# Optimization experiments

Measured on AMD Instinct MI355X. Metric: run time of the kernel, lower is better.

## Reference

```python
import jax, jax.numpy as jnp
import numpy as np

N_NODES = 50000
N_EDGES = 800000
F_IN, C1, C2, H = 256, 64, 64, 3
NEG_SLOPE = 0.2


def gat_layer(x, src, dst, W, a_src, a_dst, b, concat, num_nodes):
    """PyG-style GATConv. src/dst already include self-loops.
    W: [H*C, F_in], a_src/a_dst: [H, C], b: [H*C] or [C]."""
    H_, C_ = a_src.shape
    h = (x @ W.T).reshape(num_nodes, H_, C_)            # [N,H,C]
    al_src = (h * a_src).sum(-1)                        # [N,H]
    al_dst = (h * a_dst).sum(-1)                        # [N,H]
    e = jax.nn.leaky_relu(al_src[src] + al_dst[dst], NEG_SLOPE)  # [E,H]
    # segment softmax over incoming edges of each target node
    emax = jax.ops.segment_max(e, dst, num_segments=num_nodes)   # [N,H]
    ex = jnp.exp(e - emax[dst])
    denom = jax.ops.segment_sum(ex, dst, num_segments=num_nodes)  # [N,H]
    alpha = ex / (denom[dst] + 1e-16)                   # [E,H]
    msg = h[src] * alpha[:, :, None]                    # [E,H,C]
    out = jax.ops.segment_sum(msg, dst, num_segments=num_nodes)   # [N,H,C]
    if concat:
        return out.reshape(num_nodes, H_ * C_) + b
    return out.mean(axis=1) + b


def setup_inputs() -> dict:
    key = jax.random.key(0)
    ks = jax.random.split(key, 12)
    s = 0.05
    return {
        "x": jax.random.normal(ks[0], (N_NODES, F_IN), jnp.float32),
        "edge_index": jax.random.randint(ks[1], (2, N_EDGES), 0, N_NODES, jnp.int32),
        "W1": jax.random.normal(ks[2], (H * C1, F_IN), jnp.float32) * s,
        "a1_src": jax.random.normal(ks[3], (H, C1), jnp.float32) * s,
        "a1_dst": jax.random.normal(ks[4], (H, C1), jnp.float32) * s,
        "b1": jnp.zeros((H * C1,), jnp.float32),
        "W_mu": jax.random.normal(ks[5], (H * C2, H * C1), jnp.float32) * s,
        "a_mu_src": jax.random.normal(ks[6], (H, C2), jnp.float32) * s,
        "a_mu_dst": jax.random.normal(ks[7], (H, C2), jnp.float32) * s,
        "b_mu": jnp.zeros((C2,), jnp.float32),
        "W_lv": jax.random.normal(ks[8], (H * C2, H * C1), jnp.float32) * s,
        "a_lv_src": jax.random.normal(ks[9], (H, C2), jnp.float32) * s,
        "a_lv_dst": jax.random.normal(ks[10], (H, C2), jnp.float32) * s,
        "b_lv": jnp.zeros((C2,), jnp.float32),
    }


def reference(x, edge_index, W1, a1_src, a1_dst, b1,
              W_mu, a_mu_src, a_mu_dst, b_mu,
              W_lv, a_lv_src, a_lv_dst, b_lv):
    n = x.shape[0]
    loops = jnp.arange(n, dtype=edge_index.dtype)
    src = jnp.concatenate([edge_index[0], loops])  # add_self_loops (PyG default)
    dst = jnp.concatenate([edge_index[1], loops])
    h = gat_layer(x, src, dst, W1, a1_src, a1_dst, b1, True, n)
    h = jax.nn.relu(h)
    mu = gat_layer(h, src, dst, W_mu, a_mu_src, a_mu_dst, b_mu, False, n)
    logvar = gat_layer(h, src, dst, W_lv, a_lv_src, a_lv_dst, b_lv, False, n)
    return (mu, logvar)
```

## Files before the change

kernel.cpp:

```cpp
#include <hip/hip_runtime.h>
#include <hip/hip_bf16.h>
#include <hip/hip_fp16.h>

#define NN 50000
#define NE 800000
#define ET (NE + NN)
#define FIN 256
#define HC 192
#define NHEAD 3
#define CDIM 64
#define MAXDEG 64
#define MLW 384

typedef short short8 __attribute__((ext_vector_type(8)));
typedef float f32x4 __attribute__((ext_vector_type(4)));

__global__ __launch_bounds__(256) void hist_kernel(const int* __restrict__ ei,
                                                   int* __restrict__ cnt) {
    int e = blockIdx.x * 256 + threadIdx.x;
    if (e >= ET) return;
    int dst = (e < NE) ? ei[NE + e] : (e - NE);
    atomicAdd(&cnt[dst], 1);
}

#define SCAN_BLK 1024
__global__ __launch_bounds__(SCAN_BLK) void scan1_kernel(const int* __restrict__ cnt,
                                                         int* __restrict__ row_ptr,
                                                         int* __restrict__ partials) {
    __shared__ int sm[SCAN_BLK];
    int t = threadIdx.x;
    int g = blockIdx.x * SCAN_BLK + t;
    int v = (g < NN) ? cnt[g] : 0;
    sm[t] = v;
    __syncthreads();
    for (int off = 1; off < SCAN_BLK; off <<= 1) {
        int u = (t >= off) ? sm[t - off] : 0;
        __syncthreads();
        sm[t] += u;
        __syncthreads();
    }
    if (g < NN) row_ptr[g + 1] = sm[t];
    if (t == SCAN_BLK - 1) partials[blockIdx.x] = sm[t];
}

__global__ __launch_bounds__(64) void scan2_kernel(int* __restrict__ partials, int nb) {
    int t = threadIdx.x;
    int v = (t < nb) ? partials[t] : 0;
    int x = v;
    for (int off = 1; off < 64; off <<= 1) {
        int y = __shfl_up(x, off);
        if (t >= off) x += y;
    }
    if (t < nb) partials[t] = x - v;
}

__global__ __launch_bounds__(SCAN_BLK) void scan3_kernel(int* __restrict__ row_ptr,
                                                         const int* __restrict__ partials,
                                                         int* __restrict__ cnt) {
    int g = blockIdx.x * SCAN_BLK + threadIdx.x;
    if (g < NN) {
        row_ptr[g + 1] += partials[blockIdx.x];
        cnt[g] = 0;
    }
    if (g == 0) row_ptr[0] = 0;
}

__global__ __launch_bounds__(256) void scatter_kernel(const int* __restrict__ ei,
                                                      int* __restrict__ cnt,
                                                      const int* __restrict__ row_ptr,
                                                      int* __restrict__ csr_src) {
    int e = blockIdx.x * 256 + threadIdx.x;
    if (e >= ET) return;
    int src, dst;
    if (e < NE) { src = ei[e]; dst = ei[NE + e]; }
    else        { src = e - NE; dst = e - NE; }
    int pos = atomicAdd(&cnt[dst], 1);
    csr_src[row_ptr[dst] + pos] = src;
}

__device__ __forceinline__ unsigned short f2bf(float f) {
    unsigned int u = __float_as_uint(f);
    unsigned int r = (u + 0x7FFFu + ((u >> 16) & 1u)) >> 16;
    return (unsigned short)r;
}
__device__ __forceinline__ float bf2f(unsigned short h) {
    return __uint_as_float(((unsigned int)h) << 16);
}

#define LSTR 40
__device__ __forceinline__ void gemm_core(const float* __restrict__ A,
                                          const float* __restrict__ B1,
                                          const float* __restrict__ B2,
                                          __half* __restrict__ C,
                                          int M, int CS, int K) {
    __shared__ unsigned short Ah[128 * LSTR], Al[128 * LSTR];
    __shared__ unsigned short Bh[64 * LSTR],  Bl[64 * LSTR];

    const int tid  = threadIdx.x;
    const int lane = tid & 63;
    const int wid  = tid >> 6;
    const int wm   = wid & 1;
    const int wn   = wid >> 1;
    const int quad = lane >> 4;
    const int l15  = lane & 15;
    const int m0   = blockIdx.x * 128;
    const int n0   = blockIdx.y * 64;

    const int srow = tid >> 3;
    const int scol = (tid & 7) * 4;

    f32x4 acc[4][2];
#pragma unroll
    for (int i = 0; i < 4; i++)
#pragma unroll
        for (int j = 0; j < 2; j++) acc[i][j] = (f32x4)(0.f);

    for (int k0 = 0; k0 < K; k0 += 32) {
#pragma unroll
        for (int p = 0; p < 4; p++) {
            int r = srow + p * 32;
            int gm = m0 + r;
            float4 v = make_float4(0.f, 0.f, 0.f, 0.f);
            if (gm < M) v = *reinterpret_cast<const float4*>(&A[(size_t)gm * K + k0 + scol]);
            unsigned short h0 = f2bf(v.x), h1 = f2bf(v.y), h2 = f2bf(v.z), h3 = f2bf(v.w);
            unsigned short g0 = f2bf(v.x - bf2f(h0)), g1 = f2bf(v.y - bf2f(h1));
            unsigned short g2 = f2bf(v.z - bf2f(h2)), g3 = f2bf(v.w - bf2f(h3));
            int off = r * LSTR + scol;
            *reinterpret_cast<uint2*>(&Ah[off]) =
                make_uint2((unsigned)h0 | ((unsigned)h1 << 16), (unsigned)h2 | ((unsigned)h3 << 16));
            *reinterpret_cast<uint2*>(&Al[off]) =
                make_uint2((unsigned)g0 | ((unsigned)g1 << 16), (unsigned)g2 | ((unsigned)g3 << 16));
        }
#pragma unroll
        for (int p = 0; p < 2; p++) {
            int r = srow + p * 32;
            int r2 = n0 + r;
            const float* Brow = (r2 < 192) ? &B1[(size_t)r2 * K] : &B2[(size_t)(r2 - 192) * K];
            float4 v = *reinterpret_cast<const float4*>(&Brow[k0 + scol]);
            unsigned short h0 = f2bf(v.x), h1 = f2bf(v.y), h2 = f2bf(v.z), h3 = f2bf(v.w);
            unsigned short g0 = f2bf(v.x - bf2f(h0)), g1 = f2bf(v.y - bf2f(h1));
            unsigned short g2 = f2bf(v.z - bf2f(h2)), g3 = f2bf(v.w - bf2f(h3));
            int off = r * LSTR + scol;
            *reinterpret_cast<uint2*>(&Bh[off]) =
                make_uint2((unsigned)h0 | ((unsigned)h1 << 16), (unsigned)h2 | ((unsigned)h3 << 16));
            *reinterpret_cast<uint2*>(&Bl[off]) =
                make_uint2((unsigned)g0 | ((unsigned)g1 << 16), (unsigned)g2 | ((unsigned)g3 << 16));
        }
        __syncthreads();

        short8 afh[4], afl[4], bfh[2], bfl[2];
#pragma unroll
        for (int tm = 0; tm < 4; tm++) {
            int off = (wm * 64 + tm * 16 + l15) * LSTR + quad * 8;
            afh[tm] = *reinterpret_cast<const short8*>(&Ah[off]);
            afl[tm] = *reinterpret_cast<const short8*>(&Al[off]);
        }
#pragma unroll
        for (int tn = 0; tn < 2; tn++) {
            int off = (wn * 32 + tn * 16 + l15) * LSTR + quad * 8;
            bfh[tn] = *reinterpret_cast<const short8*>(&Bh[off]);
            bfl[tn] = *reinterpret_cast<const short8*>(&Bl[off]);
        }
#pragma unroll
        for (int tm = 0; tm < 4; tm++)
#pragma unroll
            for (int tn = 0; tn < 2; tn++) {
                acc[tm][tn] = __builtin_amdgcn_mfma_f32_16x16x32_bf16(afh[tm], bfh[tn], acc[tm][tn], 0, 0, 0);
                acc[tm][tn] = __builtin_amdgcn_mfma_f32_16x16x32_bf16(afh[tm], bfl[tn], acc[tm][tn], 0, 0, 0);
                acc[tm][tn] = __builtin_amdgcn_mfma_f32_16x16x32_bf16(afl[tm], bfh[tn], acc[tm][tn], 0, 0, 0);
            }
        __syncthreads();
    }

#pragma unroll
    for (int tm = 0; tm < 4; tm++) {
        int rbase = m0 + wm * 64 + tm * 16 + quad * 4;
#pragma unroll
        for (int r = 0; r < 4; r++) {
            int row = rbase + r;
            if (row < M) {
#pragma unroll
                for (int tn = 0; tn < 2; tn++) {
                    int col = n0 + wn * 32 + tn * 16 + l15;
                    C[(size_t)row * CS + col] = __float2half(acc[tm][tn][r]);
                }
            }
        }
    }
}

__global__ __launch_bounds__(256) void sgemm1(const float* __restrict__ A,
                                              const float* __restrict__ B,
                                              __half* __restrict__ C) {
    gemm_core(A, B, B, C, NN, HC, FIN);
}

__global__ __launch_bounds__(256) void sgemm23(const float* __restrict__ A,
                                               const float* __restrict__ Bmu,
                                               const float* __restrict__ Blv,
                                               __half* __restrict__ C) {
    gemm_core(A, Bmu, Blv, C, NN, MLW, HC);
}

__global__ __launch_bounds__(256) void al_h_kernel(const __half* __restrict__ h,
                                                   const float* __restrict__ a_src,
                                                   const float* __restrict__ a_dst,
                                                   float* __restrict__ al_src,
                                                   float* __restrict__ al_dst) {
    int wid = (blockIdx.x * 256 + threadIdx.x) >> 6;
    int lane = threadIdx.x & 63;
    if (wid >= NN * NHEAD) return;
    int n = wid / 3;
    int head = wid - n * 3;
    float v = __half2float(h[(size_t)n * HC + head * CDIM + lane]);
    float ps = v * a_src[head * CDIM + lane];
    float pd = v * a_dst[head * CDIM + lane];
#pragma unroll
    for (int off = 32; off; off >>= 1) {
        ps += __shfl_xor(ps, off);
        pd += __shfl_xor(pd, off);
    }
    if (lane == 0) { al_src[wid] = ps; al_dst[wid] = pd; }
}

__global__ __launch_bounds__(256) void al_ml_kernel(const __half* __restrict__ hml,
                                                    const float* __restrict__ amus,
                                                    const float* __restrict__ amud,
                                                    const float* __restrict__ alvs,
                                                    const float* __restrict__ alvd,
                                                    float* __restrict__ almsls,
                                                    float* __restrict__ almd,
                                                    float* __restrict__ alld) {
    int wid = (blockIdx.x * 256 + threadIdx.x) >> 6;
    int lane = threadIdx.x & 63;
    if (wid >= NN * NHEAD) return;
    int n = wid / 3;
    int head = wid - n * 3;
    int c = head * CDIM + lane;
    float vm = __half2float(hml[(size_t)n * MLW + c]);
    float vl = __half2float(hml[(size_t)n * MLW + 192 + c]);
    float ms = vm * amus[c], md = vm * amud[c];
    float ls = vl * alvs[c], ld = vl * alvd[c];
#pragma unroll
    for (int off = 32; off; off >>= 1) {
        ms += __shfl_xor(ms, off);
        md += __shfl_xor(md, off);
        ls += __shfl_xor(ls, off);
        ld += __shfl_xor(ld, off);
    }
    if (lane == 0) {
        *reinterpret_cast<float2*>(&almsls[(size_t)wid * 2]) = make_float2(ms, ls);
        almd[wid] = md;
        alld[wid] = ld;
    }
}

__device__ __forceinline__ float4 fma4h(float w, uint2 u, float4 acc) {
    asm("v_fma_mix_f32 %0, %1, %2, %0 op_sel:[0,0,0] op_sel_hi:[1,0,0]"
        : "+v"(acc.x) : "v"(u.x), "v"(w));
    asm("v_fma_mix_f32 %0, %1, %2, %0 op_sel:[1,0,0] op_sel_hi:[1,0,0]"
        : "+v"(acc.y) : "v"(u.x), "v"(w));
    asm("v_fma_mix_f32 %0, %1, %2, %0 op_sel:[0,0,0] op_sel_hi:[1,0,0]"
        : "+v"(acc.z) : "v"(u.y), "v"(w));
    asm("v_fma_mix_f32 %0, %1, %2, %0 op_sel:[1,0,0] op_sel_hi:[1,0,0]"
        : "+v"(acc.w) : "v"(u.y), "v"(w));
    return acc;
}

__global__ __launch_bounds__(192) void agg_cat_kernel(const int* __restrict__ row_ptr,
                                                      const int* __restrict__ csr_src,
                                                      const __half* __restrict__ h,
                                                      const float* __restrict__ al_src,
                                                      const float* __restrict__ al_dst,
                                                      const float* __restrict__ bias,
                                                      float* __restrict__ out) {
    __shared__ float wlds[3][64];
    int n = blockIdx.x;
    int head = threadIdx.x >> 6;
    int lane = threadIdx.x & 63;
    int start = row_ptr[n];
    int deg = row_ptr[n + 1] - start;
    float ad = al_dst[n * 3 + head];

    if (deg <= 64) {
        const int sub = lane >> 4, l16 = lane & 15;
        const int hoff = head * CDIM + l16 * 4;

        int s = 0;
        if (lane < deg) s = csr_src[start + lane];

        float ar0 = -1e30f;
        if (lane < deg) ar0 = al_src[s * 3 + head] + ad;

        int sHC = s * HC;
        uint2 pU[8];
#pragma unroll
        for (int t = 0; t < 8; ++t) {
            int e = 4 * t + sub;
            int se = __shfl(sHC, e);
            pU[t] = make_uint2(0u, 0u);
            if (e < deg) pU[t] = *reinterpret_cast<const uint2*>(&h[se + hoff]);
        }
        __builtin_amdgcn_sched_barrier(0);

        float a0 = ar0 > 0.f ? ar0 : 0.2f * ar0;
        float m = a0;
#pragma unroll
        for (int off = 32; off; off >>= 1) m = fmaxf(m, __shfl_xor(m, off));
        float ssum = 0.f;
        if (lane < deg) { float e0 = __expf(a0 - m); wlds[head][lane] = e0; ssum = e0; }
#pragma unroll
        for (int off = 32; off; off >>= 1) ssum += __shfl_xor(ssum, off);

        const float* wrow = wlds[head];
        float4 acc = make_float4(0.f, 0.f, 0.f, 0.f);
#pragma unroll
        for (int t = 0; t < 8; ++t) {
            int e = 4 * t + sub;
            float w = (e < deg) ? wrow[e] : 0.f;
            acc = fma4h(w, pU[t], acc);
        }
        for (int j = 32; j < deg; j += 4) {
            int e = j + sub;
            int se = __shfl(sHC, e);
            if (e < deg) {
                float w = wrow[e];
                uint2 u = *reinterpret_cast<const uint2*>(&h[se + hoff]);
                acc = fma4h(w, u, acc);
            }
        }
#pragma unroll
        for (int off = 16; off <= 32; off <<= 1) {
            acc.x += __shfl_xor(acc.x, off);
            acc.y += __shfl_xor(acc.y, off);
            acc.z += __shfl_xor(acc.z, off);
            acc.w += __shfl_xor(acc.w, off);
        }
        if (lane < 16) {
            float inv = 1.f / (ssum + 1e-16f);
            const float4 b4 = *reinterpret_cast<const float4*>(&bias[head * CDIM + l16 * 4]);
            float4 o;
            o.x = fmaxf(fmaf(acc.x, inv, b4.x), 0.f);
            o.y = fmaxf(fmaf(acc.y, inv, b4.y), 0.f);
            o.z = fmaxf(fmaf(acc.z, inv, b4.z), 0.f);
            o.w = fmaxf(fmaf(acc.w, inv, b4.w), 0.f);
            *reinterpret_cast<float4*>(&out[(size_t)n * HC + head * CDIM + l16 * 4]) = o;
        }
    } else {
        float m = -1e30f;
        for (int j = start + lane; j < start + deg; j += 64) {
            float a = al_src[csr_src[j] * 3 + head] + ad;
            a = a > 0.f ? a : 0.2f * a;
            m = fmaxf(m, a);
        }
#pragma unroll
        for (int off = 32; off; off >>= 1) m = fmaxf(m, __shfl_xor(m, off));
        float acc = 0.f, ssum = 0.f;
        for (int j = start; j < start + deg; ++j) {
            int s = csr_src[j];
            float a = al_src[s * 3 + head] + ad;
            a = a > 0.f ? a : 0.2f * a;
            float w = __expf(a - m);
            ssum += w;
            acc = fmaf(w, __half2float(h[(size_t)s * HC + head * CDIM + lane]), acc);
        }
        float o = acc / (ssum + 1e-16f) + bias[head * CDIM + lane];
        out[(size_t)n * HC + head * CDIM + lane] = fmaxf(o, 0.f);
    }
}

__global__ __launch_bounds__(192) void agg_mean2_kernel(const int* __restrict__ row_ptr,
                                                        const int* __restrict__ csr_src,
                                                        const __half* __restrict__ hml,
                                                        const float* __restrict__ almsls,
                                                        const float* __restrict__ almd,
                                                        const float* __restrict__ alld,
                                                        const float* __restrict__ b_mu,
                                                        const float* __restrict__ b_lv,
                                                        float* __restrict__ out) {
    __shared__ float wm_[3][64], wl_[3][64];
    __shared__ __align__(16) float red[6][64];
    int n = blockIdx.x;
    int head = threadIdx.x >> 6;
    int lane = threadIdx.x & 63;
    int start = row_ptr[n];
    int deg = row_ptr[n + 1] - start;
    float adm = almd[n * 3 + head];
    float adl = alld[n * 3 + head];

    if (deg <= 64) {
        const int sub = lane >> 4, l16 = lane & 15;
        const int hoffm = head * CDIM + l16 * 4;
        const int hoffl = hoffm + 192;

        int s = 0;
        if (lane < deg) s = csr_src[start + lane];

        float amr0 = -1e30f, avr0 = -1e30f;
        if (lane < deg) {
            float2 v = *reinterpret_cast<const float2*>(&almsls[(size_t)s * 6 + head * 2]);
            amr0 = v.x + adm;
            avr0 = v.y + adl;
        }

        int sML = s * MLW;
        uint2 pM[8], pL[8];
#pragma unroll
        for (int t = 0; t < 8; ++t) {
            int e = 4 * t + sub;
            int se = __shfl(sML, e);
            pM[t] = make_uint2(0u, 0u);
            pL[t] = make_uint2(0u, 0u);
            if (e < deg) {
                pM[t] = *reinterpret_cast<const uint2*>(&hml[se + hoffm]);
                pL[t] = *reinterpret_cast<const uint2*>(&hml[se + hoffl]);
            }
        }
        __builtin_amdgcn_sched_barrier(0);

        float am0 = amr0 > 0.f ? amr0 : 0.2f * amr0;
        float av0 = avr0 > 0.f ? avr0 : 0.2f * avr0;
        float mm = am0, ml = av0;
#pragma unroll
        for (int off = 32; off; off >>= 1) {
            mm = fmaxf(mm, __shfl_xor(mm, off));
            ml = fmaxf(ml, __shfl_xor(ml, off));
        }
        float sm = 0.f, sl = 0.f;
        if (lane < deg) {
            float em = __expf(am0 - mm); wm_[head][lane] = em; sm = em;
            float el = __expf(av0 - ml); wl_[head][lane] = el; sl = el;
        }
#pragma unroll
        for (int off = 32; off; off >>= 1) {
            sm += __shfl_xor(sm, off);
            sl += __shfl_xor(sl, off);
        }

        float4 am4 = make_float4(0.f, 0.f, 0.f, 0.f);
        float4 al4 = make_float4(0.f, 0.f, 0.f, 0.f);
#pragma unroll
        for (int t = 0; t < 8; ++t) {
            int e = 4 * t + sub;
            float wmA = 0.f, wlA = 0.f;
            if (e < deg) { wmA = wm_[head][e]; wlA = wl_[head][e]; }
            am4 = fma4h(wmA, pM[t], am4);
            al4 = fma4h(wlA, pL[t], al4);
        }
        for (int j = 32; j < deg; j += 4) {
            int e = j + sub;
            int se = __shfl(sML, e);
            if (e < deg) {
                float wmA = wm_[head][e], wlA = wl_[head][e];
                uint2 uM = *reinterpret_cast<const uint2*>(&hml[se + hoffm]);
                uint2 uL = *reinterpret_cast<const uint2*>(&hml[se + hoffl]);
                am4 = fma4h(wmA, uM, am4);
                al4 = fma4h(wlA, uL, al4);
            }
        }
#pragma unroll
        for (int off = 16; off <= 32; off <<= 1) {
            am4.x += __shfl_xor(am4.x, off); am4.y += __shfl_xor(am4.y, off);
            am4.z += __shfl_xor(am4.z, off); am4.w += __shfl_xor(am4.w, off);
            al4.x += __shfl_xor(al4.x, off); al4.y += __shfl_xor(al4.y, off);
            al4.z += __shfl_xor(al4.z, off); al4.w += __shfl_xor(al4.w, off);
        }
        if (lane < 16) {
            float invm = 1.f / (sm + 1e-16f);
            float invl = 1.f / (sl + 1e-16f);
            float4 rm, rl;
            rm.x = am4.x * invm; rm.y = am4.y * invm; rm.z = am4.z * invm; rm.w = am4.w * invm;
            rl.x = al4.x * invl; rl.y = al4.y * invl; rl.z = al4.z * invl; rl.w = al4.w * invl;
            *reinterpret_cast<float4*>(&red[head][l16 * 4]) = rm;
            *reinterpret_cast<float4*>(&red[3 + head][l16 * 4]) = rl;
        }
    } else {
        for (int pass = 0; pass < 2; ++pass) {
            float ad = pass ? adl : adm;
            int coff = pass ? 192 : 0;
            float m = -1e30f;
            for (int j = start + lane; j < start + deg; j += 64) {
                float a = almsls[(size_t)csr_src[j] * 6 + head * 2 + pass] + ad;
                a = a > 0.f ? a : 0.2f * a;
                m = fmaxf(m, a);
            }
#pragma unroll
            for (int off = 32; off; off >>= 1) m = fmaxf(m, __shfl_xor(m, off));
            float acc = 0.f, ssum = 0.f;
            for (int j = start; j < start + deg; ++j) {
                int s = csr_src[j];
                float a = almsls[(size_t)s * 6 + head * 2 + pass] + ad;
                a = a > 0.f ? a : 0.2f * a;
                float w = __expf(a - m);
                ssum += w;
                acc = fmaf(w, __half2float(hml[(size_t)s * MLW + coff + head * CDIM + lane]), acc);
            }
            red[pass * 3 + head][lane] = acc / (ssum + 1e-16f);
        }
    }
    __syncthreads();
    if (threadIdx.x < 64) {
        out[(size_t)n * CDIM + lane] =
            (red[0][lane] + red[1][lane] + red[2][lane]) * (1.f / 3.f) + b_mu[lane];
    } else if (threadIdx.x < 128) {
        out[(size_t)NN * CDIM + (size_t)n * CDIM + lane] =
            (red[3][lane] + red[4][lane] + red[5][lane]) * (1.f / 3.f) + b_lv[lane];
    }
}

extern "C" void kernel_launch(void* const* d_in, const int* in_sizes, int n_in,
                              void* d_out, int out_size, void* d_ws, size_t ws_size,
                              hipStream_t stream) {
    const float* x    = (const float*)d_in[0];
    const int*   ei   = (const int*)d_in[1];
    const float* W1   = (const float*)d_in[2];
    const float* a1s  = (const float*)d_in[3];
    const float* a1d  = (const float*)d_in[4];
    const float* b1   = (const float*)d_in[5];
    const float* Wmu  = (const float*)d_in[6];
    const float* amus = (const float*)d_in[7];
    const float* amud = (const float*)d_in[8];
    const float* bmu  = (const float*)d_in[9];
    const float* Wlv  = (const float*)d_in[10];
    const float* alvs = (const float*)d_in[11];
    const float* alvd = (const float*)d_in[12];
    const float* blv  = (const float*)d_in[13];
    float* out = (float*)d_out;

    size_t off = 0;
    auto carve = [&](size_t bytes) {
        void* p = (char*)d_ws + off;
        off += (bytes + 255) & ~(size_t)255;
        return p;
    };
    int*    cnt      = (int*)carve((size_t)NN * 4);
    int*    row_ptr  = (int*)carve((size_t)(NN + 1) * 4);
    int*    partials = (int*)carve(64 * 4);
    int*    csr      = (int*)carve((size_t)ET * 4);
    __half* h1f16    = (__half*)carve((size_t)NN * HC * 2);
    float*  hrelu    = (float*)carve((size_t)NN * HC * 4);
    __half* hml      = (__half*)carve((size_t)NN * MLW * 2);
    float*  al1s     = (float*)carve((size_t)NN * 3 * 4);
    float*  al1d     = (float*)carve((size_t)NN * 3 * 4);
    float*  almsls   = (float*)carve((size_t)NN * 6 * 4);
    float*  almd     = (float*)carve((size_t)NN * 3 * 4);
    float*  alld     = (float*)carve((size_t)NN * 3 * 4);

    const int scan_blocks = (NN + SCAN_BLK - 1) / SCAN_BLK;

    hipMemsetAsync(cnt, 0, (size_t)NN * 4, stream);
    hist_kernel<<<(ET + 255) / 256, 256, 0, stream>>>(ei, cnt);
    scan1_kernel<<<scan_blocks, SCAN_BLK, 0, stream>>>(cnt, row_ptr, partials);
    scan2_kernel<<<1, 64, 0, stream>>>(partials, scan_blocks);
    scan3_kernel<<<scan_blocks, SCAN_BLK, 0, stream>>>(row_ptr, partials, cnt);
    scatter_kernel<<<(ET + 255) / 256, 256, 0, stream>>>(ei, cnt, row_ptr, csr);

    dim3 g1((NN + 127) / 128, HC / 64);
    sgemm1<<<g1, 256, 0, stream>>>(x, W1, h1f16);
    al_h_kernel<<<(NN * 3 + 3) / 4, 256, 0, stream>>>(h1f16, a1s, a1d, al1s, al1d);
    agg_cat_kernel<<<NN, 192, 0, stream>>>(row_ptr, csr, h1f16, al1s, al1d, b1, hrelu);

    dim3 g2((NN + 127) / 128, MLW / 64);
    sgemm23<<<g2, 256, 0, stream>>>(hrelu, Wmu, Wlv, hml);
    al_ml_kernel<<<(NN * 3 + 3) / 4, 256, 0, stream>>>(hml, amus, amud, alvs, alvd,
                                                       almsls, almd, alld);
    agg_mean2_kernel<<<NN, 192, 0, stream>>>(row_ptr, csr, hml,
                                             almsls, almd, alld, bmu, blv, out);
}
```

Measured before the change: 500.3 us.

## Fuse attention logit projections into GEMM epilogues and specialize aggregation by degree

The per-head attention dot products (al_src/al_dst) are now computed inside the GEMM epilogue, using shuffle and shared-memory reductions over each 64-column head tile. This removes the two separate al kernels and their re-read of the fp16 feature matrices. The mean-layer aggregation fast path is also templated on how many 4-edge blocks to prefetch (4, 6 or 8), so low-degree nodes issue fewer predicated loads and hold fewer registers. In exchange the GEMM epilogue gets extra shuffles, a shared-memory buffer and a block barrier, and three template instantiations add code size.

```diff
diff --git a/kernel.cpp b/kernel.cpp
--- a/kernel.cpp
+++ b/kernel.cpp
@@ -9,7 +9,6 @@
 #define HC 192
 #define NHEAD 3
 #define CDIM 64
-#define MAXDEG 64
 #define MLW 384
 
 typedef short short8 __attribute__((ext_vector_type(8)));
@@ -92,9 +91,14 @@
                                           const float* __restrict__ B1,
                                           const float* __restrict__ B2,
                                           __half* __restrict__ C,
-                                          int M, int CS, int K) {
+                                          int M, int CS, int K,
+                                          const float* __restrict__ as_seg,
+                                          const float* __restrict__ ad_seg,
+                                          float* __restrict__ os, int os_stride,
+                                          float* __restrict__ od, int od_stride) {
     __shared__ unsigned short Ah[128 * LSTR], Al[128 * LSTR];
     __shared__ unsigned short Bh[64 * LSTR],  Bl[64 * LSTR];
+    __shared__ float sred_s[2][128], sred_d[2][128];
 
     const int tid  = threadIdx.x;
     const int lane = tid & 63;
@@ -172,87 +176,83 @@
         __syncthreads();
     }
 
+    const float a_s0 = as_seg[wn * 32 + l15];
+    const float a_s1 = as_seg[wn * 32 + 16 + l15];
+    const float a_d0 = ad_seg[wn * 32 + l15];
+    const float a_d1 = ad_seg[wn * 32 + 16 + l15];
+    const int col0 = n0 + wn * 32 + l15;
+    const int col1 = col0 + 16;
+
 #pragma unroll
     for (int tm = 0; tm < 4; tm++) {
-        int rbase = m0 + wm * 64 + tm * 16 + quad * 4;
+        int rloc0 = wm * 64 + tm * 16 + quad * 4;
 #pragma unroll
         for (int r = 0; r < 4; r++) {
-            int row = rbase + r;
+            int rloc = rloc0 + r;
+            int row = m0 + rloc;
+            __half hv0 = __float2half(acc[tm][0][r]);
+            __half hv1 = __float2half(acc[tm][1][r]);
+            float f0 = __half2float(hv0);
+            float f1 = __half2float(hv1);
+            float ps = f0 * a_s0 + f1 * a_s1;
+            float pd = f0 * a_d0 + f1 * a_d1;
+#pragma unroll
+            for (int off = 8; off; off >>= 1) {
+                ps += __shfl_xor(ps, off);
+                pd += __shfl_xor(pd, off);
+            }
+            if (l15 == 0) {
+                sred_s[wn][rloc] = ps;
+                sred_d[wn][rloc] = pd;
+            }
             if (row < M) {
-#pragma unroll
-                for (int tn = 0; tn < 2; tn++) {
-                    int col = n0 + wn * 32 + tn * 16 + l15;
-                    C[(size_t)row * CS + col] = __float2half(acc[tm][tn][r]);
-                }
-            }
+                C[(size_t)row * CS + col0] = hv0;
+                C[(size_t)row * CS + col1] = hv1;
+            }
+        }
+    }
+    __syncthreads();
+    if (tid < 128) {
+        int row = m0 + tid;
+        if (row < M) {
+            os[(size_t)row * os_stride] = sred_s[0][tid] + sred_s[1][tid];
+            od[(size_t)row * od_stride] = sred_d[0][tid] + sred_d[1][tid];
         }
     }
 }
 
 __global__ __launch_bounds__(256) void sgemm1(const float* __restrict__ A,
                                               const float* __restrict__ B,
-                                              __half* __restrict__ C) {
-    gemm_core(A, B, B, C, NN, HC, FIN);
+                                              __half* __restrict__ C,
+                                              const float* __restrict__ a_src,
+                                              const float* __restrict__ a_dst,
+                                              float* __restrict__ al_src,
+                                              float* __restrict__ al_dst) {
+    int head = blockIdx.y;
+    gemm_core(A, B, B, C, NN, HC, FIN,
+              a_src + head * 64, a_dst + head * 64,
+              al_src + head, 3, al_dst + head, 3);
 }
 
 __global__ __launch_bounds__(256) void sgemm23(const float* __restrict__ A,
                                                const float* __restrict__ Bmu,
                                                const float* __restrict__ Blv,
-                                               __half* __restrict__ C) {
-    gemm_core(A, Bmu, Blv, C, NN, MLW, HC);
-}
-
-__global__ __launch_bounds__(256) void al_h_kernel(const __half* __restrict__ h,
-                                                   const float* __restrict__ a_src,
-                                                   const float* __restrict__ a_dst,
-                                                   float* __restrict__ al_src,
-                                                   float* __restrict__ al_dst) {
-    int wid = (blockIdx.x * 256 + threadIdx.x) >> 6;
-    int lane = threadIdx.x & 63;
-    if (wid >= NN * NHEAD) return;
-    int n = wid / 3;
-    int head = wid - n * 3;
-    float v = __half2float(h[(size_t)n * HC + head * CDIM + lane]);
-    float ps = v * a_src[head * CDIM + lane];
-    float pd = v * a_dst[head * CDIM + lane];
-#pragma unroll
-    for (int off = 32; off; off >>= 1) {
-        ps += __shfl_xor(ps, off);
-        pd += __shfl_xor(pd, off);
-    }
-    if (lane == 0) { al_src[wid] = ps; al_dst[wid] = pd; }
-}
-
-__global__ __launch_bounds__(256) void al_ml_kernel(const __half* __restrict__ hml,
-                                                    const float* __restrict__ amus,
-                                                    const float* __restrict__ amud,
-                                                    const float* __restrict__ alvs,
-                                                    const float* __restrict__ alvd,
-                                                    float* __restrict__ almsls,
-                                                    float* __restrict__ almd,
-                                                    float* __restrict__ alld) {
-    int wid = (blockIdx.x * 256 + threadIdx.x) >> 6;
-    int lane = threadIdx.x & 63;
-    if (wid >= NN * NHEAD) return;
-    int n = wid / 3;
-    int head = wid - n * 3;
-    int c = head * CDIM + lane;
-    float vm = __half2float(hml[(size_t)n * MLW + c]);
-    float vl = __half2float(hml[(size_t)n * MLW + 192 + c]);
-    float ms = vm * amus[c], md = vm * amud[c];
-    float ls = vl * alvs[c], ld = vl * alvd[c];
-#pragma unroll
-    for (int off = 32; off; off >>= 1) {
-        ms += __shfl_xor(ms, off);
-        md += __shfl_xor(md, off);
-        ls += __shfl_xor(ls, off);
-        ld += __shfl_xor(ld, off);
-    }
-    if (lane == 0) {
-        *reinterpret_cast<float2*>(&almsls[(size_t)wid * 2]) = make_float2(ms, ls);
-        almd[wid] = md;
-        alld[wid] = ld;
-    }
+                                               __half* __restrict__ C,
+                                               const float* __restrict__ amus,
+                                               const float* __restrict__ amud,
+                                               const float* __restrict__ alvs,
+                                               const float* __restrict__ alvd,
+                                               float* __restrict__ almsls,
+                                               float* __restrict__ almd,
+                                               float* __restrict__ alld) {
+    int seg = blockIdx.y;
+    bool lv = seg >= 3;
+    int hd = lv ? seg - 3 : seg;
+    const float* as_ = (lv ? alvs : amus) + hd * 64;
+    const float* ad_ = (lv ? alvd : amud) + hd * 64;
+    float* os = almsls + hd * 2 + (lv ? 1 : 0);
+    float* od = (lv ? alld : almd) + hd;
+    gemm_core(A, Bmu, Blv, C, NN, MLW, HC, as_, ad_, os, 6, od, 3);
 }
 
 __device__ __forceinline__ float4 fma4h(float w, uint2 u, float4 acc) {
@@ -366,6 +366,91 @@
         }
         float o = acc / (ssum + 1e-16f) + bias[head * CDIM + lane];
         out[(size_t)n * HC + head * CDIM + lane] = fmaxf(o, 0.f);
+    }
+}
+
+template <int NBLK>
+__device__ __forceinline__ void ml_fast(int deg, int head, int lane, int s,
+                                        float amr0, float avr0,
+                                        const __half* __restrict__ hml,
+                                        float (&wm_)[3][64], float (&wl_)[3][64],
+                                        float (&red)[6][64]) {
+    const int sub = lane >> 4, l16 = lane & 15;
+    const int hoffm = head * CDIM + l16 * 4;
+    const int hoffl = hoffm + 192;
+    int sML = s * MLW;
+
+    uint2 pM[NBLK], pL[NBLK];
+#pragma unroll
+    for (int t = 0; t < NBLK; ++t) {
+        int e = 4 * t + sub;
+        int se = __shfl(sML, e);
+        pM[t] = make_uint2(0u, 0u);
+        pL[t] = make_uint2(0u, 0u);
+        if (e < deg) {
+            pM[t] = *reinterpret_cast<const uint2*>(&hml[se + hoffm]);
+            pL[t] = *reinterpret_cast<const uint2*>(&hml[se + hoffl]);
+        }
+    }
+    __builtin_amdgcn_sched_barrier(0);
+
+    float am0 = amr0 > 0.f ? amr0 : 0.2f * amr0;
+    float av0 = avr0 > 0.f ? avr0 : 0.2f * avr0;
+    float mm = am0, ml = av0;
+#pragma unroll
+    for (int off = 32; off; off >>= 1) {
+        mm = fmaxf(mm, __shfl_xor(mm, off));
+        ml = fmaxf(ml, __shfl_xor(ml, off));
+    }
+    float sm = 0.f, sl = 0.f;
+    if (lane < deg) {
+        float em = __expf(am0 - mm); wm_[head][lane] = em; sm = em;
+        float el = __expf(av0 - ml); wl_[head][lane] = el; sl = el;
+    }
+#pragma unroll
+    for (int off = 32; off; off >>= 1) {
+        sm += __shfl_xor(sm, off);
+        sl += __shfl_xor(sl, off);
+    }
+
+    float4 am4 = make_float4(0.f, 0.f, 0.f, 0.f);
+    float4 al4 = make_float4(0.f, 0.f, 0.f, 0.f);
+#pragma unroll
+    for (int t = 0; t < NBLK; ++t) {
+        int e = 4 * t + sub;
+        float wmA = 0.f, wlA = 0.f;
+        if (e < deg) { wmA = wm_[head][e]; wlA = wl_[head][e]; }
+        am4 = fma4h(wmA, pM[t], am4);
+        al4 = fma4h(wlA, pL[t], al4);
+    }
+    if constexpr (NBLK == 8) {
+        for (int j = 32; j < deg; j += 4) {
+            int e = j + sub;
+            int se = __shfl(sML, e);
+            if (e < deg) {
+                float wmA = wm_[head][e], wlA = wl_[head][e];
+                uint2 uM = *reinterpret_cast<const uint2*>(&hml[se + hoffm]);
+                uint2 uL = *reinterpret_cast<const uint2*>(&hml[se + hoffl]);
+                am4 = fma4h(wmA, uM, am4);
+                al4 = fma4h(wlA, uL, al4);
+            }
+        }
+    }
+#pragma unroll
+    for (int off = 16; off <= 32; off <<= 1) {
+        am4.x += __shfl_xor(am4.x, off); am4.y += __shfl_xor(am4.y, off);
+        am4.z += __shfl_xor(am4.z, off); am4.w += __shfl_xor(am4.w, off);
+        al4.x += __shfl_xor(al4.x, off); al4.y += __shfl_xor(al4.y, off);
+        al4.z += __shfl_xor(al4.z, off); al4.w += __shfl_xor(al4.w, off);
+    }
+    if (lane < 16) {
+        float invm = 1.f / (sm + 1e-16f);
+        float invl = 1.f / (sl + 1e-16f);
+        float4 rm, rl;
+        rm.x = am4.x * invm; rm.y = am4.y * invm; rm.z = am4.z * invm; rm.w = am4.w * invm;
+        rl.x = al4.x * invl; rl.y = al4.y * invl; rl.z = al4.z * invl; rl.w = al4.w * invl;
+        *reinterpret_cast<float4*>(&red[head][l16 * 4]) = rm;
+        *reinterpret_cast<float4*>(&red[3 + head][l16 * 4]) = rl;
     }
 }
 
@@ -389,13 +474,8 @@
     float adl = alld[n * 3 + head];
 
     if (deg <= 64) {
-        const int sub = lane >> 4, l16 = lane & 15;
-        const int hoffm = head * CDIM + l16 * 4;
-        const int hoffl = hoffm + 192;
-
         int s = 0;
         if (lane < deg) s = csr_src[start + lane];
-
         float amr0 = -1e30f, avr0 = -1e30f;
         if (lane < deg) {
             float2 v = *reinterpret_cast<const float2*>(&almsls[(size_t)s * 6 + head * 2]);
@@ -403,77 +483,9 @@
             avr0 = v.y + adl;
         }
 
-        int sML = s * MLW;
-        uint2 pM[8], pL[8];
-#pragma unroll
-        for (int t = 0; t < 8; ++t) {
-            int e = 4 * t + sub;
-            int se = __shfl(sML, e);
-            pM[t] = make_uint2(0u, 0u);
-            pL[t] = make_uint2(0u, 0u);
-            if (e < deg) {
-                pM[t] = *reinterpret_cast<const uint2*>(&hml[se + hoffm]);
-                pL[t] = *reinterpret_cast<const uint2*>(&hml[se + hoffl]);
-            }
-        }
-        __builtin_amdgcn_sched_barrier(0);
-
-        float am0 = amr0 > 0.f ? amr0 : 0.2f * amr0;
-        float av0 = avr0 > 0.f ? avr0 : 0.2f * avr0;
-        float mm = am0, ml = av0;
-#pragma unroll
-        for (int off = 32; off; off >>= 1) {
-            mm = fmaxf(mm, __shfl_xor(mm, off));
-            ml = fmaxf(ml, __shfl_xor(ml, off));
-        }
-        float sm = 0.f, sl = 0.f;
-        if (lane < deg) {
-            float em = __expf(am0 - mm); wm_[head][lane] = em; sm = em;
-            float el = __expf(av0 - ml); wl_[head][lane] = el; sl = el;
-        }
-#pragma unroll
-        for (int off = 32; off; off >>= 1) {
-            sm += __shfl_xor(sm, off);
-            sl += __shfl_xor(sl, off);
-        }
-
-        float4 am4 = make_float4(0.f, 0.f, 0.f, 0.f);
-        float4 al4 = make_float4(0.f, 0.f, 0.f, 0.f);
-#pragma unroll
-        for (int t = 0; t < 8; ++t) {
-            int e = 4 * t + sub;
-            float wmA = 0.f, wlA = 0.f;
-            if (e < deg) { wmA = wm_[head][e]; wlA = wl_[head][e]; }
-            am4 = fma4h(wmA, pM[t], am4);
-            al4 = fma4h(wlA, pL[t], al4);
-        }
-        for (int j = 32; j < deg; j += 4) {
-            int e = j + sub;
-            int se = __shfl(sML, e);
-            if (e < deg) {
-                float wmA = wm_[head][e], wlA = wl_[head][e];
-                uint2 uM = *reinterpret_cast<const uint2*>(&hml[se + hoffm]);
-                uint2 uL = *reinterpret_cast<const uint2*>(&hml[se + hoffl]);
-                am4 = fma4h(wmA, uM, am4);
-                al4 = fma4h(wlA, uL, al4);
-            }
-        }
-#pragma unroll
-        for (int off = 16; off <= 32; off <<= 1) {
-            am4.x += __shfl_xor(am4.x, off); am4.y += __shfl_xor(am4.y, off);
-            am4.z += __shfl_xor(am4.z, off); am4.w += __shfl_xor(am4.w, off);
-            al4.x += __shfl_xor(al4.x, off); al4.y += __shfl_xor(al4.y, off);
-            al4.z += __shfl_xor(al4.z, off); al4.w += __shfl_xor(al4.w, off);
-        }
-        if (lane < 16) {
-            float invm = 1.f / (sm + 1e-16f);
-            float invl = 1.f / (sl + 1e-16f);
-            float4 rm, rl;
-            rm.x = am4.x * invm; rm.y = am4.y * invm; rm.z = am4.z * invm; rm.w = am4.w * invm;
-            rl.x = al4.x * invl; rl.y = al4.y * invl; rl.z = al4.z * invl; rl.w = al4.w * invl;
-            *reinterpret_cast<float4*>(&red[head][l16 * 4]) = rm;
-            *reinterpret_cast<float4*>(&red[3 + head][l16 * 4]) = rl;
-        }
+        if (deg <= 16)      ml_fast<4>(deg, head, lane, s, amr0, avr0, hml, wm_, wl_, red);
+        else if (deg <= 24) ml_fast<6>(deg, head, lane, s, amr0, avr0, hml, wm_, wl_, red);
+        else                ml_fast<8>(deg, head, lane, s, amr0, avr0, hml, wm_, wl_, red);
     } else {
         for (int pass = 0; pass < 2; ++pass) {
             float ad = pass ? adl : adm;
@@ -556,14 +568,12 @@
     scatter_kernel<<<(ET + 255) / 256, 256, 0, stream>>>(ei, cnt, row_ptr, csr);
 
     dim3 g1((NN + 127) / 128, HC / 64);
-    sgemm1<<<g1, 256, 0, stream>>>(x, W1, h1f16);
-    al_h_kernel<<<(NN * 3 + 3) / 4, 256, 0, stream>>>(h1f16, a1s, a1d, al1s, al1d);
+    sgemm1<<<g1, 256, 0, stream>>>(x, W1, h1f16, a1s, a1d, al1s, al1d);
     agg_cat_kernel<<<NN, 192, 0, stream>>>(row_ptr, csr, h1f16, al1s, al1d, b1, hrelu);
 
     dim3 g2((NN + 127) / 128, MLW / 64);
-    sgemm23<<<g2, 256, 0, stream>>>(hrelu, Wmu, Wlv, hml);
-    al_ml_kernel<<<(NN * 3 + 3) / 4, 256, 0, stream>>>(hml, amus, amud, alvs, alvd,
-                                                       almsls, almd, alld);
+    sgemm23<<<g2, 256, 0, stream>>>(hrelu, Wmu, Wlv, hml, amus, amud, alvs, alvd,
+                                    almsls, almd, alld);
     agg_mean2_kernel<<<NN, 192, 0, stream>>>(row_ptr, csr, hml,
                                              almsls, almd, alld, bmu, blv, out);
 }
```

After: 482.2 us. -3.6%, faster.
